# Performance work log

Measured on AMD Instinct MI355X. Metric: run time of the kernel, lower is better.

## Reference

```python
import jax, jax.numpy as jnp
import numpy as np

ND, NT, B = 16384, 16384, 4096
FD, FT, C = 256, 256, 768


def _gat(x_src, x_dst, ei, Ws, Wd, a_s, a_d, b, num_dst, self_loops):
    """PyG GATConv, heads=1: per-edge attention softmax over incoming edges."""
    if self_loops:
        loops = jnp.arange(num_dst, dtype=ei.dtype)
        ei = jnp.concatenate([ei, jnp.stack([loops, loops])], axis=1)
    src, dst = ei[0], ei[1]
    hs = x_src @ Ws                                   # [Ns, C]
    hd = x_dst @ Wd                                   # [Ndst, C]
    e = jax.nn.leaky_relu((hs @ a_s)[src] + (hd @ a_d)[dst], 0.2)   # [E]
    m = jax.ops.segment_max(e, dst, num_segments=num_dst)
    p = jnp.exp(e - m[dst])
    s = jax.ops.segment_sum(p, dst, num_segments=num_dst)
    alpha = p / (s[dst] + 1e-16)
    out = jax.ops.segment_sum(hs[src] * alpha[:, None], dst, num_segments=num_dst)
    return out + b


def _l2norm(x):
    n = jnp.linalg.norm(x, axis=1, keepdims=True)
    return x / jnp.maximum(n, 1e-12)


def setup_inputs() -> dict:
    ks = iter(jax.random.split(jax.random.key(0), 64))
    def nrm(shape, fan_in=None):
        s = 1.0 if fan_in is None else (1.0 / fan_in) ** 0.5
        return jax.random.normal(next(ks), shape, jnp.float32) * s
    inp = {}
    inp["x_drug"] = nrm((ND, FD))
    inp["x_target"] = nrm((NT, FT))
    inp["cell_features"] = nrm((B, 890))
    for et, fs, fd in (("dd", FD, FD), ("dt", FD, FT), ("tt", FT, FT)):
        inp[f"W_src_{et}"] = nrm((fs, C), fs)
        inp[f"W_dst_{et}"] = nrm((fd, C), fd)
        inp[f"a_src_{et}"] = nrm((C,), C)
        inp[f"a_dst_{et}"] = nrm((C,), C)
        inp[f"b_{et}"] = jnp.zeros((C,), jnp.float32)
    for name, fi, fo in (("red1", 890, 2048), ("red2", 2048, 512), ("red3", 512, 2 * C),
                         ("r2a", 4 * C, 2048), ("r2b", 2048, 512), ("r2c", 512, C), ("cls", C, 2)):
        inp[f"{name}_w"] = nrm((fi, fo), fi)
        inp[f"{name}_b"] = jnp.zeros((fo,), jnp.float32)
    inp["drug1_id"] = jax.random.randint(next(ks), (B,), 0, ND)
    inp["drug2_id"] = jax.random.randint(next(ks), (B,), 0, ND)
    inp["ei_dd"] = jax.random.randint(next(ks), (2, 131072), 0, ND)
    inp["ei_dt"] = jnp.stack([jax.random.randint(next(ks), (262144,), 0, ND),
                              jax.random.randint(next(ks), (262144,), 0, NT)])
    inp["ei_tt"] = jax.random.randint(next(ks), (2, 262144), 0, NT)
    return inp


def reference(x_drug, x_target, cell_features,
              W_src_dd, W_dst_dd, a_src_dd, a_dst_dd, b_dd,
              W_src_dt, W_dst_dt, a_src_dt, a_dst_dt, b_dt,
              W_src_tt, W_dst_tt, a_src_tt, a_dst_tt, b_tt,
              red1_w, red1_b, red2_w, red2_b, red3_w, red3_b,
              r2a_w, r2a_b, r2b_w, r2b_b, r2c_w, r2c_b,
              cls_w, cls_b,
              drug1_id, drug2_id, ei_dd, ei_dt, ei_tt):
    # HeteroConv (aggr='sum') followed by per-type ReLU, num_layers=1
    drug = jax.nn.relu(_gat(x_drug, x_drug, ei_dd,
                            W_src_dd, W_dst_dd, a_src_dd, a_dst_dd, b_dd, ND, True))
    target = jax.nn.relu(
        _gat(x_drug, x_target, ei_dt, W_src_dt, W_dst_dt, a_src_dt, a_dst_dt, b_dt, NT, False)
        + _gat(x_target, x_target, ei_tt, W_src_tt, W_dst_tt, a_src_tt, a_dst_tt, b_tt, NT, True))
    del target  # with num_layers=1 the target embeddings never feed the output (faithful)
    d1 = drug[drug1_id]
    d2 = drug[drug2_id]
    cell = _l2norm(cell_features)
    cell = jax.nn.relu(cell @ red1_w + red1_b)
    cell = jax.nn.relu(cell @ red2_w + red2_b)
    cell = jax.nn.relu(cell @ red3_w + red3_b)          # [B, 2*C]
    hidden = _l2norm(jnp.concatenate([d1, d2, cell], axis=1))  # [B, 4*C]
    hidden = jax.nn.relu(hidden @ r2a_w + r2a_b)
    hidden = jax.nn.relu(hidden @ r2b_w + r2b_b)
    hidden = jax.nn.relu(hidden @ r2c_w + r2c_b)
    return hidden @ cls_w + cls_b                       # [B, 2]
```

## Files before the change

### kernel.cpp

```cpp
#include <hip/hip_runtime.h>
#include <cstdint>

#define ND 16384
#define BATCH 4096
#define CDIM 768
#define E_DD 131072
#define FD 256

typedef unsigned short u16;
typedef u16 u16x4 __attribute__((ext_vector_type(4)));
typedef u16 u16x8 __attribute__((ext_vector_type(8)));
typedef short s16x8 __attribute__((ext_vector_type(8)));
typedef float f32x4 __attribute__((ext_vector_type(4)));

__device__ __forceinline__ u16 f2bf(float x) {
  union { float f; uint32_t u; } v; v.f = x;
  uint32_t r = v.u + 0x7fffu + ((v.u >> 16) & 1u);
  return (u16)(r >> 16);
}
__device__ __forceinline__ float bf2f(u16 h) {
  union { float f; uint32_t u; } v; v.u = ((uint32_t)h) << 16;
  return v.f;
}
__device__ __forceinline__ uint32_t split2p(float x) {
  u16 h = f2bf(x);
  u16 l = f2bf(x - bf2f(h));
  return ((uint32_t)h << 16) | l;
}

#define GLOAD_LDS16(gp, lp)                                                   \
  __builtin_amdgcn_global_load_lds(                                           \
      (__attribute__((address_space(1))) void*)(gp),                          \
      (__attribute__((address_space(3))) void*)(lp), 16, 0, 0)

__device__ __forceinline__ int xcd_chunk(int f, int nwg) {
  int q = nwg >> 3, r = nwg & 7;
  int xcd = f & 7, s = f >> 3;
  return (xcd < r ? xcd * (q + 1) : r * (q + 1) + (xcd - r) * q) + s;
}

#define KP 40

template <int KS, int OUT_BF16, int RELU, int BIAS, int ASPLIT, int ALO, int BLO,
          int BKD>
__device__ __forceinline__ void gemm_core(
    int bx, int by, int bz,
    const float* __restrict__ Af,
    const u16* __restrict__ Ahi, const u16* __restrict__ Alo,
    const u16* __restrict__ Bhi, const u16* __restrict__ Blo,
    const float* __restrict__ bias,
    float* __restrict__ Cf, u16* __restrict__ Chi,
    int M, int N, int K, u16* AsB, u16* BsB) {
  constexpr int MT = 4, NT = 4;
  constexpr int BM = 128, BN = 128;
  constexpr int ASEG = BM / 64;
  constexpr int BSEG = BN / 64;
  constexpr bool DIRECT = (ASPLIT == 0 && ALO == 0 && BLO == 0);

  const int t = threadIdx.x;
  const int bm0 = bx * BM, bn0 = by * BN;
  const int wid = t >> 6, lane = t & 63;
  const int quad = lane >> 4, l16 = lane & 15;
  const int wm0 = (wid >> 1) * (MT * 16);
  const int wn0 = (wid & 1) * (NT * 16);

  const int chunk = K / KS;
  const int kbeg = (KS > 1) ? bz * chunk : 0;
  const int kend = kbeg + chunk;

  float bvv[NT];
#pragma unroll
  for (int ni = 0; ni < NT; ++ni)
    bvv[ni] = BIAS ? bias[bn0 + wn0 + ni * 16 + l16] : 0.f;

  f32x4 acc[MT][NT];
#pragma unroll
  for (int i = 0; i < MT; ++i)
#pragma unroll
    for (int j = 0; j < NT; ++j) acc[i][j] = (f32x4){0.f, 0.f, 0.f, 0.f};

  if constexpr (DIRECT) {
    constexpr int SLOTS = BKD / 8;
    constexpr int SM = SLOTS - 1;
    constexpr int NLD = (BM * BKD) / (256 * 8);
    auto stageA = [&](int buf, int kk) {
#pragma unroll
      for (int c = 0; c < NLD; ++c) {
        int s = t + 256 * c;
        int r = s / SLOTS, j = s % SLOTS;
        int jj = j ^ (r & SM);
        size_t goff = (size_t)(bm0 + r) * K + kk + jj * 8;
        int lofs = __builtin_amdgcn_readfirstlane((wid * 64 + 256 * c) * 8);
        GLOAD_LDS16(Ahi + goff, AsB + buf * (BM * BKD) + lofs);
      }
    };
    auto stageB = [&](int buf, int kk) {
#pragma unroll
      for (int c = 0; c < NLD; ++c) {
        int s = t + 256 * c;
        int r = s / SLOTS, j = s % SLOTS;
        int jj = j ^ (r & SM);
        size_t goff = (size_t)(bn0 + r) * K + kk + jj * 8;
        int lofs = __builtin_amdgcn_readfirstlane((wid * 64 + 256 * c) * 8);
        GLOAD_LDS16(Bhi + goff, BsB + buf * (BN * BKD) + lofs);
      }
    };
    const int rsw = l16 & SM;
    stageA(0, kbeg);
    stageB(0, kbeg);
    int cur = 0;
    for (int k0 = kbeg;;) {
      __syncthreads();
      int kn = k0 + BKD;
      if (kn < kend) {
        stageA(cur ^ 1, kn);
        stageB(cur ^ 1, kn);
      }
      const u16* Ab = AsB + cur * (BM * BKD);
      const u16* Bb = BsB + cur * (BN * BKD);
#pragma unroll
      for (int h = 0; h < BKD / 32; ++h) {
        s16x8 ah[MT], bh[NT];
#pragma unroll
        for (int mi = 0; mi < MT; ++mi)
          ah[mi] = *(const s16x8*)(Ab + (wm0 + mi * 16 + l16) * BKD +
                                   (((h * 4 + quad) ^ rsw) * 8));
#pragma unroll
        for (int ni = 0; ni < NT; ++ni)
          bh[ni] = *(const s16x8*)(Bb + (wn0 + ni * 16 + l16) * BKD +
                                   (((h * 4 + quad) ^ rsw) * 8));
#pragma unroll
        for (int mi = 0; mi < MT; ++mi)
#pragma unroll
          for (int ni = 0; ni < NT; ++ni)
            acc[mi][ni] = __builtin_amdgcn_mfma_f32_16x16x32_bf16(
                ah[mi], bh[ni], acc[mi][ni], 0, 0, 0);
      }
      k0 = kn;
      cur ^= 1;
      if (k0 >= kend) break;
    }
  } else {
    auto As = [&](int a, int r, int k) -> u16& { return AsB[(a * BM + r) * KP + k]; };
    auto Bs = [&](int a, int r, int k) -> u16& { return BsB[(a * BN + r) * KP + k]; };

    u16x8 pAh[ASEG], pAl[ASEG], pBh[BSEG], pBl[BSEG];

    auto loadA = [&](int c, int kk) {
      int s = t + 256 * c, row = s >> 2, kq = (s & 3) * 8;
      size_t off = (size_t)(bm0 + row) * K + kk + kq;
      if (ASPLIT) {
        f32x4 v0 = *(const f32x4*)(Af + off);
        f32x4 v1 = *(const f32x4*)(Af + off + 4);
        u16x8 h, l;
#pragma unroll
        for (int e = 0; e < 4; ++e) {
          uint32_t p = split2p(v0[e]);
          h[e] = (u16)(p >> 16); l[e] = (u16)(p & 0xffffu);
          uint32_t q = split2p(v1[e]);
          h[e + 4] = (u16)(q >> 16); l[e + 4] = (u16)(q & 0xffffu);
        }
        pAh[c] = h; pAl[c] = l;
      } else {
        pAh[c] = *(const u16x8*)(Ahi + off);
        if (ALO) pAl[c] = *(const u16x8*)(Alo + off);
      }
    };
    auto loadB = [&](int c, int kk) {
      int s = t + 256 * c, row = s >> 2, kq = (s & 3) * 8;
      size_t off = (size_t)(bn0 + row) * K + kk + kq;
      pBh[c] = *(const u16x8*)(Bhi + off);
      if (BLO) pBl[c] = *(const u16x8*)(Blo + off);
    };

#pragma unroll
    for (int c = 0; c < ASEG; ++c) loadA(c, kbeg);
#pragma unroll
    for (int c = 0; c < BSEG; ++c) loadB(c, kbeg);

    for (int k0 = kbeg;;) {
      __syncthreads();
#pragma unroll
      for (int c = 0; c < ASEG; ++c) {
        int s = t + 256 * c, row = s >> 2, kq = (s & 3) * 8;
        *(u16x8*)&As(0, row, kq) = pAh[c];
        if (ALO) *(u16x8*)&As(1, row, kq) = pAl[c];
      }
#pragma unroll
      for (int c = 0; c < BSEG; ++c) {
        int s = t + 256 * c, row = s >> 2, kq = (s & 3) * 8;
        *(u16x8*)&Bs(0, row, kq) = pBh[c];
        if (BLO) *(u16x8*)&Bs(1, row, kq) = pBl[c];
      }
      __syncthreads();

      int kn = k0 + 32;
      if (kn < kend) {
#pragma unroll
        for (int c = 0; c < ASEG; ++c) loadA(c, kn);
#pragma unroll
        for (int c = 0; c < BSEG; ++c) loadB(c, kn);
      }

      s16x8 ah[MT], al[MT], bh[NT], bl[NT];
#pragma unroll
      for (int mi = 0; mi < MT; ++mi) {
        ah[mi] = *(const s16x8*)&As(0, wm0 + mi * 16 + l16, quad * 8);
        if (ALO) al[mi] = *(const s16x8*)&As(1, wm0 + mi * 16 + l16, quad * 8);
      }
#pragma unroll
      for (int ni = 0; ni < NT; ++ni) {
        bh[ni] = *(const s16x8*)&Bs(0, wn0 + ni * 16 + l16, quad * 8);
        if (BLO) bl[ni] = *(const s16x8*)&Bs(1, wn0 + ni * 16 + l16, quad * 8);
      }
#pragma unroll
      for (int mi = 0; mi < MT; ++mi)
#pragma unroll
        for (int ni = 0; ni < NT; ++ni) {
          acc[mi][ni] = __builtin_amdgcn_mfma_f32_16x16x32_bf16(
              ah[mi], bh[ni], acc[mi][ni], 0, 0, 0);
          if (BLO)
            acc[mi][ni] = __builtin_amdgcn_mfma_f32_16x16x32_bf16(
                ah[mi], bl[ni], acc[mi][ni], 0, 0, 0);
          if (ALO)
            acc[mi][ni] = __builtin_amdgcn_mfma_f32_16x16x32_bf16(
                al[mi], bh[ni], acc[mi][ni], 0, 0, 0);
        }
      k0 = kn;
      if (k0 >= kend) break;
    }
  }

  float* Cp = (KS > 1) ? Cf + (size_t)bz * M * N : Cf;
#pragma unroll
  for (int mi = 0; mi < MT; ++mi) {
#pragma unroll
    for (int ni = 0; ni < NT; ++ni) {
      int row = bm0 + wm0 + mi * 16 + quad * 4;
      int col = bn0 + wn0 + ni * 16 + l16;
#pragma unroll
      for (int r = 0; r < 4; ++r) {
        float v = acc[mi][ni][r] + bvv[ni];
        if (RELU) v = fmaxf(v, 0.f);
        size_t o = (size_t)(row + r) * N + col;
        if (OUT_BF16) Chi[o] = f2bf(v);
        else Cp[o] = v;
      }
    }
  }
}

template <int KS, int OUT_BF16, int RELU, int BIAS, int ASPLIT, int ALO, int BLO,
          int BKD>
__global__ __launch_bounds__(256) void mfma_gemm(
    const float* __restrict__ Af,
    const u16* __restrict__ Ahi, const u16* __restrict__ Alo,
    const u16* __restrict__ Bhi, const u16* __restrict__ Blo,
    const float* __restrict__ bias,
    float* __restrict__ Cf, u16* __restrict__ Chi,
    int M, int N, int K) {
  constexpr bool DIRECT = (ASPLIT == 0 && ALO == 0 && BLO == 0);
  __shared__ __align__(16) u16 AsB[DIRECT ? 2 * 128 * BKD : (ALO ? 2 : 1) * 128 * KP];
  __shared__ __align__(16) u16 BsB[DIRECT ? 2 * 128 * BKD : (BLO ? 2 : 1) * 128 * KP];
  int f = blockIdx.x + gridDim.x * blockIdx.y;
  int wg = xcd_chunk(f, gridDim.x * gridDim.y);
  int bx = wg % gridDim.x, by = wg / gridDim.x;
  gemm_core<KS, OUT_BF16, RELU, BIAS, ASPLIT, ALO, BLO, BKD>(
      bx, by, (KS > 1) ? (int)blockIdx.z : 0,
      Af, Ahi, Alo, Bhi, Blo, bias, Cf, Chi, M, N, K, AsB, BsB);
}

__device__ __forceinline__ void gat_body(
    int idx, int t,
    const u16* __restrict__ hs, const float* __restrict__ es,
    const float* __restrict__ ed, const int* __restrict__ offsets,
    const int* __restrict__ slots, const float* __restrict__ bias,
    const int* __restrict__ list, const int* __restrict__ cnt,
    u16* __restrict__ out) {
  if (idx >= *cnt) return;
  int d = list[idx];
  int lane = t & 63;
  int beg = offsets[d], end = offsets[d + 1];
  float edv = ed[d];
  float mx = -1e30f;
  for (int j = beg + lane; j < end; j += 64) {
    float e = es[slots[j]] + edv;
    e = e >= 0.f ? e : 0.2f * e;
    mx = fmaxf(mx, e);
  }
#pragma unroll
  for (int m = 32; m; m >>= 1) mx = fmaxf(mx, __shfl_xor(mx, m));
  float sm = 0.f;
  for (int j = beg + lane; j < end; j += 64) {
    float e = es[slots[j]] + edv;
    e = e >= 0.f ? e : 0.2f * e;
    sm += expf(e - mx);
  }
#pragma unroll
  for (int m = 32; m; m >>= 1) sm += __shfl_xor(sm, m);
  float inv = 1.f / (sm + 1e-16f);
  int c8 = lane * 8;
  int c4 = 512 + lane * 4;
  float a8[8] = {};
  float a4[4] = {};
  for (int j = beg; j < end; ++j) {
    int srcn = slots[j];
    float e = es[srcn] + edv;
    e = e >= 0.f ? e : 0.2f * e;
    float alpha = expf(e - mx) * inv;
    const u16* hrow = hs + (size_t)srcn * CDIM;
    u16x8 r8 = *(const u16x8*)(hrow + c8);
    u16x4 r4 = *(const u16x4*)(hrow + c4);
#pragma unroll
    for (int e2 = 0; e2 < 8; ++e2) a8[e2] = fmaf(alpha, bf2f(r8[e2]), a8[e2]);
#pragma unroll
    for (int e2 = 0; e2 < 4; ++e2) a4[e2] = fmaf(alpha, bf2f(r4[e2]), a4[e2]);
  }
  u16* orow = out + (size_t)d * CDIM;
  u16x8 o8;
  u16x4 o4;
#pragma unroll
  for (int e2 = 0; e2 < 8; ++e2) o8[e2] = f2bf(fmaxf(a8[e2] + bias[c8 + e2], 0.f));
#pragma unroll
  for (int e2 = 0; e2 < 4; ++e2) o4[e2] = f2bf(fmaxf(a4[e2] + bias[c4 + e2], 0.f));
  *(u16x8*)(orow + c8) = o8;
  *(u16x4*)(orow + c4) = o4;
}

__global__ __launch_bounds__(256) void gat_aggregate(
    const u16* __restrict__ hs, const float* __restrict__ es,
    const float* __restrict__ ed, const int* __restrict__ offsets,
    const int* __restrict__ slots, const float* __restrict__ bias,
    const int* __restrict__ list, const int* __restrict__ cnt,
    u16* __restrict__ out) {
  gat_body(blockIdx.x * 4 + (threadIdx.x >> 6), threadIdx.x,
           hs, es, ed, offsets, slots, bias, list, cnt, out);
}

__global__ __launch_bounds__(256) void dual_gemm_red1_hs_scatter(
    const u16* __restrict__ cn, const u16* __restrict__ r1T,
    const float* __restrict__ red1_b, u16* __restrict__ c1,
    const float* __restrict__ xd, const u16* __restrict__ wsrcT,
    u16* __restrict__ hs,
    const int* __restrict__ src, const int* __restrict__ dst,
    int* __restrict__ cursor, int* __restrict__ slots) {
  __shared__ __align__(16) u16 SMEM[16384];
  int b = blockIdx.x;
  if (b < 512) {
    int wg = xcd_chunk(b, 512);
    gemm_core<1, 1, 1, 1, 0, 0, 0, 32>(wg & 31, wg >> 5, 0, nullptr, cn, nullptr,
                                       r1T, nullptr, red1_b, nullptr, c1,
                                       BATCH, 2048, 896, SMEM, SMEM + 2 * 128 * 32);
  } else if (b < 1280) {
    int b2 = b - 512;
    gemm_core<1, 1, 0, 0, 1, 1, 0, 32>(b2 & 127, b2 >> 7, 0, xd, nullptr, nullptr,
                                       wsrcT, nullptr, nullptr, nullptr, hs,
                                       ND, CDIM, FD, SMEM, SMEM + 2 * 128 * KP);
  } else {
    int e = (b - 1280) * 256 + threadIdx.x;
    if (e < E_DD) {
      int pos = atomicAdd(&cursor[dst[e]], 1);
      slots[pos] = src[e];
    }
  }
}

template <int KS>
__global__ void reduce_split_ks(const float* __restrict__ P,
                                const float* __restrict__ bias,
                                u16* __restrict__ Chi, int M, int N) {
  int i = blockIdx.x * 256 + threadIdx.x;
  int total = (M * N) >> 2;
  if (i >= total) return;
  f32x4 s = ((const f32x4*)P)[i];
#pragma unroll
  for (int z = 1; z < KS; ++z) s += ((const f32x4*)P)[(size_t)z * total + i];
  int col = (i * 4) % N;
  f32x4 bv = *(const f32x4*)(bias + col);
  u16x4 h;
#pragma unroll
  for (int e = 0; e < 4; ++e) h[e] = f2bf(fmaxf(s[e] + bv[e], 0.f));
  *(u16x4*)&Chi[i * 4] = h;
}

__global__ void reduce_cls(const float* __restrict__ P,
                           const float* __restrict__ bias,
                           const float* __restrict__ clsw,
                           const float* __restrict__ clsb,
                           float* __restrict__ out) {
  int row = blockIdx.x * 4 + (threadIdx.x >> 6);
  int lane = threadIdx.x & 63;
  const f32x4* p0 = (const f32x4*)(P + (size_t)row * CDIM);
  const f32x4* p1 = (const f32x4*)(P + (size_t)BATCH * CDIM + (size_t)row * CDIM);
  float s0 = 0.f, s1 = 0.f;
#pragma unroll
  for (int i = 0; i < 3; ++i) {
    int c4 = lane + 64 * i;
    f32x4 a = p0[c4] + p1[c4];
    f32x4 bv = *(const f32x4*)(bias + c4 * 4);
#pragma unroll
    for (int e = 0; e < 4; ++e) {
      float h = fmaxf(a[e] + bv[e], 0.f);
      int c = c4 * 4 + e;
      s0 = fmaf(h, clsw[c * 2 + 0], s0);
      s1 = fmaf(h, clsw[c * 2 + 1], s1);
    }
  }
#pragma unroll
  for (int m = 32; m; m >>= 1) {
    s0 += __shfl_xor(s0, m);
    s1 += __shfl_xor(s1, m);
  }
  if (lane == 0) {
    out[row * 2 + 0] = s0 + clsb[0];
    out[row * 2 + 1] = s1 + clsb[1];
  }
}

struct TDesc {
  const float* W;
  u16* Th;
  int K, N, Kpad, start;
};
struct TPack { TDesc d[7]; };

#define P1_T 11328
#define P1_W (P1_T + 256)
#define P1_I (P1_W + 64)
__global__ __launch_bounds__(256) void prep1(
    TPack p,
    const float* __restrict__ Wsrc, const float* __restrict__ Wdst,
    const float* __restrict__ a_s, const float* __restrict__ a_d,
    float* __restrict__ wsv, float* __restrict__ wdv,
    int* __restrict__ counts, int* __restrict__ mask, int* __restrict__ cnt,
    const float* __restrict__ cellf, u16* __restrict__ cn_hi) {
  __shared__ __align__(16) float S[1088];
  int b = blockIdx.x;
  int t = threadIdx.x;
  if (b < P1_T) {
    float (*tile)[33] = (float(*)[33])S;
    int mi = 0;
#pragma unroll
    for (int i = 1; i < 7; ++i)
      if (b >= p.d[i].start) mi = i;
    TDesc dd = p.d[mi];
    int rel = b - dd.start;
    int tilesX = dd.Kpad / 32;
    int k0 = (rel % tilesX) * 32, n0 = (rel / tilesX) * 32;
    int tx = t & 31, ty = t >> 5;
#pragma unroll
    for (int i = 0; i < 4; ++i) {
      int k = k0 + ty + 8 * i, n = n0 + tx;
      tile[ty + 8 * i][tx] = (k < dd.K && n < dd.N) ? dd.W[(size_t)k * dd.N + n] : 0.f;
    }
    __syncthreads();
#pragma unroll
    for (int i = 0; i < 4; ++i) {
      int n = n0 + ty + 8 * i, k = k0 + tx;
      if (n < dd.N) dd.Th[(size_t)n * dd.Kpad + k] = f2bf(tile[tx][ty + 8 * i]);
    }
  } else if (b < P1_W) {
    int k = b - P1_T;
    float* rs = S;
    float* rd = S + 256;
    float s = 0.f, d = 0.f;
    for (int c = t; c < CDIM; c += 256) {
      s += Wsrc[(size_t)k * CDIM + c] * a_s[c];
      d += Wdst[(size_t)k * CDIM + c] * a_d[c];
    }
    rs[t] = s; rd[t] = d;
    __syncthreads();
    for (int st = 128; st; st >>= 1) {
      if (t < st) { rs[t] += rs[t + st]; rd[t] += rd[t + st]; }
      __syncthreads();
    }
    if (t == 0) { wsv[k] = rs[0]; wdv[k] = rd[0]; }
  } else if (b < P1_I) {
    int i = (b - P1_W) * 256 + t;
    if (i < ND) { counts[i] = 1; mask[i] = 0; }
    if (i == 0) *cnt = 0;
  } else {
    int row = b - P1_I;
    float* red = S;
    const float* irow = cellf + (size_t)row * 890;
    float s = 0.f;
    for (int c = t; c < 890; c += 256) { float v = irow[c]; s += v * v; }
    red[t] = s;
    __syncthreads();
    for (int st = 128; st; st >>= 1) {
      if (t < st) red[t] += red[t + st];
      __syncthreads();
    }
    float inv = 1.f / fmaxf(sqrtf(red[0]), 1e-12f);
    for (int c = t; c < 896; c += 256) {
      float v = (c < 890) ? irow[c] * inv : 0.f;
      cn_hi[(size_t)row * 896 + c] = f2bf(v);
    }
  }
}

#define P2_E (ND * FD / 1024)
#define P2_M (P2_E + BATCH / 256)
__global__ __launch_bounds__(256) void prep2(
    const float* __restrict__ x, const float* __restrict__ wsv,
    const float* __restrict__ wdv, float* __restrict__ es, float* __restrict__ ed,
    const int* __restrict__ d1, const int* __restrict__ d2, int* __restrict__ mask,
    const int* __restrict__ dst, int* __restrict__ counts) {
  int b = blockIdx.x, t = threadIdx.x;
  if (b < P2_E) {
    int i = b * 256 + t;
    int lane = t & 63;
    int row = i >> 6;
    int c4 = lane * 4;
    f32x4 v = ((const f32x4*)x)[i];
    f32x4 ws = *(const f32x4*)(wsv + c4);
    f32x4 wd = *(const f32x4*)(wdv + c4);
    float a = v[0] * ws[0] + v[1] * ws[1] + v[2] * ws[2] + v[3] * ws[3];
    float bb = v[0] * wd[0] + v[1] * wd[1] + v[2] * wd[2] + v[3] * wd[3];
#pragma unroll
    for (int m = 32; m; m >>= 1) {
      a += __shfl_xor(a, m);
      bb += __shfl_xor(bb, m);
    }
    if (lane == 0) { es[row] = a; ed[row] = bb; }
  } else if (b < P2_M) {
    int i = (b - P2_E) * 256 + t;
    mask[d1[i]] = 1;
    mask[d2[i]] = 1;
  } else {
    int e = (b - P2_M) * 256 + t;
    atomicAdd(&counts[dst[e]], 1);
  }
}

__global__ __launch_bounds__(512) void prep3(
    const int* __restrict__ mask, int* __restrict__ cnt, int* __restrict__ list,
    const int* __restrict__ counts, int* __restrict__ offsets,
    int* __restrict__ cursor, int* __restrict__ slots) {
  __shared__ int part[512];
  int b = blockIdx.x, t = threadIdx.x;
  if (b < 32) {
    int i = b * 512 + t;
    if (mask[i]) {
      int pos = atomicAdd(cnt, 1);
      list[pos] = i;
    }
  } else {
    int base = t * 32;
    int s = 0;
    for (int i = 0; i < 32; ++i) s += counts[base + i];
    part[t] = s;
    __syncthreads();
    if (t == 0) {
      int run = 0;
      for (int i = 0; i < 512; ++i) { int tmp = part[i]; part[i] = run; run += tmp; }
      offsets[ND] = run;
    }
    __syncthreads();
    int run = part[t];
    for (int i = 0; i < 32; ++i) {
      int d = base + i;
      offsets[d] = run;
      slots[run] = d;
      cursor[d] = run + 1;
      run += counts[d];
    }
  }
}

__global__ __launch_bounds__(256) void hidden_build_bf16(
    const u16* __restrict__ drug, const u16* __restrict__ c3,
    const int* __restrict__ d1, const int* __restrict__ d2,
    u16* __restrict__ hhi) {
  int row = blockIdx.x;
  int t = threadIdx.x;
  const u16* s1 = drug + (size_t)d1[row] * CDIM;
  const u16* s2 = drug + (size_t)d2[row] * CDIM;
  const u16* s3 = c3 + (size_t)row * (2 * CDIM);
  float vals[12];
  float ss = 0.f;
#pragma unroll
  for (int i = 0; i < 12; ++i) {
    int c = t + 256 * i;
    float v;
    if (i < 3)      v = bf2f(s1[c]);
    else if (i < 6) v = bf2f(s2[c - CDIM]);
    else            v = bf2f(s3[c - 2 * CDIM]);
    vals[i] = v;
    ss += v * v;
  }
  __shared__ float red[256];
  red[t] = ss;
  __syncthreads();
  for (int st = 128; st; st >>= 1) {
    if (t < st) red[t] += red[t + st];
    __syncthreads();
  }
  float inv = 1.f / fmaxf(sqrtf(red[0]), 1e-12f);
  u16* hrow_h = hhi + (size_t)row * (4 * CDIM);
#pragma unroll
  for (int i = 0; i < 12; ++i) hrow_h[t + 256 * i] = f2bf(vals[i] * inv);
}

extern "C" void kernel_launch(void* const* d_in, const int* in_sizes, int n_in,
                              void* d_out, int out_size, void* d_ws, size_t ws_size,
                              hipStream_t stream) {
  const float* x_drug   = (const float*)d_in[0];
  const float* cellf    = (const float*)d_in[2];
  const float* W_src_dd = (const float*)d_in[3];
  const float* W_dst_dd = (const float*)d_in[4];
  const float* a_src_dd = (const float*)d_in[5];
  const float* a_dst_dd = (const float*)d_in[6];
  const float* b_dd     = (const float*)d_in[7];
  const float* red1_w = (const float*)d_in[18];
  const float* red1_b = (const float*)d_in[19];
  const float* red2_w = (const float*)d_in[20];
  const float* red2_b = (const float*)d_in[21];
  const float* red3_w = (const float*)d_in[22];
  const float* red3_b = (const float*)d_in[23];
  const float* r2a_w  = (const float*)d_in[24];
  const float* r2a_b  = (const float*)d_in[25];
  const float* r2b_w  = (const float*)d_in[26];
  const float* r2b_b  = (const float*)d_in[27];
  const float* r2c_w  = (const float*)d_in[28];
  const float* r2c_b  = (const float*)d_in[29];
  const float* cls_w  = (const float*)d_in[30];
  const float* cls_b  = (const float*)d_in[31];
  const int* drug1_id = (const int*)d_in[32];
  const int* drug2_id = (const int*)d_in[33];
  const int* ei_dd    = (const int*)d_in[34];
  float* out = (float*)d_out;

  const int* dd_src = ei_dd;
  const int* dd_dst = ei_dd + E_DD;

  char* w = (char*)d_ws;
  size_t off = 0;
  auto alloc = [&](size_t bytes) -> char* {
    char* p = w + off;
    off = (off + bytes + 255) & ~(size_t)255;
    return p;
  };
  u16* hs   = (u16*)alloc((size_t)ND * CDIM * 2);
  u16* drug = (u16*)alloc((size_t)ND * CDIM * 2);
  u16* c3   = (u16*)alloc((size_t)BATCH * 2 * CDIM * 2);
  float* P  = (float*)alloc((size_t)4 * BATCH * 512 * 4);
  u16* hid_hi = hs;
  u16* cn_hi = (u16*)alloc((size_t)BATCH * 896 * 2);
  u16* c1_hi = (u16*)alloc((size_t)BATCH * 2048 * 2);
  u16* c2_hi = (u16*)alloc((size_t)BATCH * 512 * 2);
  u16* wsrcT_hi = (u16*)alloc((size_t)CDIM * FD * 2);
  u16* r1T_hi = (u16*)alloc((size_t)2048 * 896 * 2);
  u16* r2T_hi = (u16*)alloc((size_t)512 * 2048 * 2);
  u16* r3T_hi = (u16*)alloc((size_t)1536 * 512 * 2);
  u16* raT_hi = (u16*)alloc((size_t)2048 * 3072 * 2);
  u16* rbT_hi = (u16*)alloc((size_t)512 * 2048 * 2);
  u16* rcT_hi = (u16*)alloc((size_t)768 * 512 * 2);
  float* es  = (float*)alloc((size_t)ND * 4);
  float* ed  = (float*)alloc((size_t)ND * 4);
  float* wsv = (float*)alloc(FD * 4);
  float* wdv = (float*)alloc(FD * 4);
  int* counts  = (int*)alloc((size_t)ND * 4);
  int* offsets = (int*)alloc((size_t)(ND + 1) * 4);
  int* cursor  = (int*)alloc((size_t)ND * 4);
  int* slots   = (int*)alloc((size_t)(E_DD + ND) * 4);
  int* mask    = (int*)alloc((size_t)ND * 4);
  int* list    = (int*)alloc((size_t)ND * 4);
  int* cnt     = (int*)alloc(256);
  (void)ws_size; (void)n_in; (void)in_sizes; (void)out_size;

  TPack tp;
  tp.d[0] = {W_src_dd, wsrcT_hi, 256, 768, 256, 0};
  tp.d[1] = {red1_w, r1T_hi, 890, 2048, 896, 192};
  tp.d[2] = {red2_w, r2T_hi, 2048, 512, 2048, 1984};
  tp.d[3] = {red3_w, r3T_hi, 512, 1536, 512, 3008};
  tp.d[4] = {r2a_w, raT_hi, 3072, 2048, 3072, 3776};
  tp.d[5] = {r2b_w, rbT_hi, 2048, 512, 2048, 9920};
  tp.d[6] = {r2c_w, rcT_hi, 512, 768, 512, 10944};
  prep1<<<15744, 256, 0, stream>>>(tp, W_src_dd, W_dst_dd, a_src_dd, a_dst_dd,
                                   wsv, wdv, counts, mask, cnt, cellf, cn_hi);

  prep2<<<4624, 256, 0, stream>>>(x_drug, wsv, wdv, es, ed, drug1_id, drug2_id,
                                  mask, dd_dst, counts);

  prep3<<<33, 512, 0, stream>>>(mask, cnt, list, counts, offsets, cursor, slots);

  dual_gemm_red1_hs_scatter<<<1792, 256, 0, stream>>>(
      cn_hi, r1T_hi, red1_b, c1_hi, x_drug, wsrcT_hi, hs,
      dd_src, dd_dst, cursor, slots);

  mfma_gemm<4, 0, 0, 0, 0, 0, 0, 64><<<dim3(BATCH / 128, 512 / 128, 4), 256, 0, stream>>>(
      nullptr, c1_hi, nullptr, r2T_hi, nullptr, nullptr, P, nullptr, BATCH, 512, 2048);
  reduce_split_ks<4><<<BATCH * 512 / 1024, 256, 0, stream>>>(P, red2_b, c2_hi, BATCH, 512);
  mfma_gemm<1, 1, 1, 1, 0, 0, 0, 64><<<dim3(BATCH / 128, 1536 / 128), 256, 0, stream>>>(
      nullptr, c2_hi, nullptr, r3T_hi, nullptr, red3_b, nullptr, c3, BATCH, 1536, 512);

  gat_aggregate<<<ND / 4, 256, 0, stream>>>(hs, es, ed, offsets, slots, b_dd, list, cnt, drug);

  hidden_build_bf16<<<BATCH, 256, 0, stream>>>(drug, c3, drug1_id, drug2_id, hid_hi);

  mfma_gemm<1, 1, 1, 1, 0, 0, 0, 64><<<dim3(BATCH / 128, 2048 / 128), 256, 0, stream>>>(
      nullptr, hid_hi, nullptr, raT_hi, nullptr, r2a_b, nullptr, c1_hi, BATCH, 2048, 3072);
  mfma_gemm<4, 0, 0, 0, 0, 0, 0, 64><<<dim3(BATCH / 128, 512 / 128, 4), 256, 0, stream>>>(
      nullptr, c1_hi, nullptr, rbT_hi, nullptr, nullptr, P, nullptr, BATCH, 512, 2048);
  reduce_split_ks<4><<<BATCH * 512 / 1024, 256, 0, stream>>>(P, r2b_b, c2_hi, BATCH, 512);
  mfma_gemm<2, 0, 0, 0, 0, 0, 0, 64><<<dim3(BATCH / 128, CDIM / 128, 2), 256, 0, stream>>>(
      nullptr, c2_hi, nullptr, rcT_hi, nullptr, nullptr, P, nullptr, BATCH, CDIM, 512);
  reduce_cls<<<BATCH / 4, 256, 0, stream>>>(P, r2c_b, cls_w, cls_b, out);
}
```

Measured before the change: 452.3 us.

## Use 8-wave workgroups for standalone GEMMs and drop XCD tile remapping

Generalizes the GEMM core over the wave count, so standalone GEMM launches run 512 threads with 8 waves in a 2x4 layout, each wave computing a 64x32 sub-tile. This halves per-wave accumulator registers and spreads the staging loads across more threads, aiming for better latency hiding. It also removes the XCD-aware block-index remap from both the standalone and fused GEMMs and uses raw block indices instead. That can hurt L2 locality across chiplets, and each wave now reuses less data per fragment load.

```diff
diff --git a/kernel.cpp b/kernel.cpp
--- a/kernel.cpp
+++ b/kernel.cpp
@@ -33,16 +33,10 @@
       (__attribute__((address_space(1))) void*)(gp),                          \
       (__attribute__((address_space(3))) void*)(lp), 16, 0, 0)
 
-__device__ __forceinline__ int xcd_chunk(int f, int nwg) {
-  int q = nwg >> 3, r = nwg & 7;
-  int xcd = f & 7, s = f >> 3;
-  return (xcd < r ? xcd * (q + 1) : r * (q + 1) + (xcd - r) * q) + s;
-}
-
 #define KP 40
 
 template <int KS, int OUT_BF16, int RELU, int BIAS, int ASPLIT, int ALO, int BLO,
-          int BKD>
+          int BKD, int NW>
 __device__ __forceinline__ void gemm_core(
     int bx, int by, int bz,
     const float* __restrict__ Af,
@@ -51,7 +45,10 @@
     const float* __restrict__ bias,
     float* __restrict__ Cf, u16* __restrict__ Chi,
     int M, int N, int K, u16* AsB, u16* BsB) {
-  constexpr int MT = 4, NT = 4;
+  constexpr int NTH = NW * 64;
+  constexpr int WC = (NW == 8) ? 4 : 2;
+  constexpr int MT = 4;
+  constexpr int NT = (NW == 8) ? 2 : 4;
   constexpr int BM = 128, BN = 128;
   constexpr int ASEG = BM / 64;
   constexpr int BSEG = BN / 64;
@@ -61,8 +58,8 @@
   const int bm0 = bx * BM, bn0 = by * BN;
   const int wid = t >> 6, lane = t & 63;
   const int quad = lane >> 4, l16 = lane & 15;
-  const int wm0 = (wid >> 1) * (MT * 16);
-  const int wn0 = (wid & 1) * (NT * 16);
+  const int wm0 = (wid / WC) * (MT * 16);
+  const int wn0 = (wid % WC) * (NT * 16);
 
   const int chunk = K / KS;
   const int kbeg = (KS > 1) ? bz * chunk : 0;
@@ -82,26 +79,26 @@
   if constexpr (DIRECT) {
     constexpr int SLOTS = BKD / 8;
     constexpr int SM = SLOTS - 1;
-    constexpr int NLD = (BM * BKD) / (256 * 8);
+    constexpr int NLD = (BM * BKD) / (NTH * 8);
     auto stageA = [&](int buf, int kk) {
 #pragma unroll
       for (int c = 0; c < NLD; ++c) {
-        int s = t + 256 * c;
+        int s = t + NTH * c;
         int r = s / SLOTS, j = s % SLOTS;
         int jj = j ^ (r & SM);
         size_t goff = (size_t)(bm0 + r) * K + kk + jj * 8;
-        int lofs = __builtin_amdgcn_readfirstlane((wid * 64 + 256 * c) * 8);
+        int lofs = __builtin_amdgcn_readfirstlane((wid * 64 + NTH * c) * 8);
         GLOAD_LDS16(Ahi + goff, AsB + buf * (BM * BKD) + lofs);
       }
     };
     auto stageB = [&](int buf, int kk) {
 #pragma unroll
       for (int c = 0; c < NLD; ++c) {
-        int s = t + 256 * c;
+        int s = t + NTH * c;
         int r = s / SLOTS, j = s % SLOTS;
         int jj = j ^ (r & SM);
         size_t goff = (size_t)(bn0 + r) * K + kk + jj * 8;
-        int lofs = __builtin_amdgcn_readfirstlane((wid * 64 + 256 * c) * 8);
+        int lofs = __builtin_amdgcn_readfirstlane((wid * 64 + NTH * c) * 8);
         GLOAD_LDS16(Bhi + goff, BsB + buf * (BN * BKD) + lofs);
       }
     };
@@ -251,8 +248,8 @@
 }
 
 template <int KS, int OUT_BF16, int RELU, int BIAS, int ASPLIT, int ALO, int BLO,
-          int BKD>
-__global__ __launch_bounds__(256) void mfma_gemm(
+          int BKD, int NW>
+__global__ __launch_bounds__(NW * 64) void mfma_gemm(
     const float* __restrict__ Af,
     const u16* __restrict__ Ahi, const u16* __restrict__ Alo,
     const u16* __restrict__ Bhi, const u16* __restrict__ Blo,
@@ -262,11 +259,8 @@
   constexpr bool DIRECT = (ASPLIT == 0 && ALO == 0 && BLO == 0);
   __shared__ __align__(16) u16 AsB[DIRECT ? 2 * 128 * BKD : (ALO ? 2 : 1) * 128 * KP];
   __shared__ __align__(16) u16 BsB[DIRECT ? 2 * 128 * BKD : (BLO ? 2 : 1) * 128 * KP];
-  int f = blockIdx.x + gridDim.x * blockIdx.y;
-  int wg = xcd_chunk(f, gridDim.x * gridDim.y);
-  int bx = wg % gridDim.x, by = wg / gridDim.x;
-  gemm_core<KS, OUT_BF16, RELU, BIAS, ASPLIT, ALO, BLO, BKD>(
-      bx, by, (KS > 1) ? (int)blockIdx.z : 0,
+  gemm_core<KS, OUT_BF16, RELU, BIAS, ASPLIT, ALO, BLO, BKD, NW>(
+      blockIdx.x, blockIdx.y, (KS > 1) ? (int)blockIdx.z : 0,
       Af, Ahi, Alo, Bhi, Blo, bias, Cf, Chi, M, N, K, AsB, BsB);
 }
 
@@ -347,15 +341,14 @@
   __shared__ __align__(16) u16 SMEM[16384];
   int b = blockIdx.x;
   if (b < 512) {
-    int wg = xcd_chunk(b, 512);
-    gemm_core<1, 1, 1, 1, 0, 0, 0, 32>(wg & 31, wg >> 5, 0, nullptr, cn, nullptr,
-                                       r1T, nullptr, red1_b, nullptr, c1,
-                                       BATCH, 2048, 896, SMEM, SMEM + 2 * 128 * 32);
+    gemm_core<1, 1, 1, 1, 0, 0, 0, 32, 4>(b & 31, b >> 5, 0, nullptr, cn, nullptr,
+                                          r1T, nullptr, red1_b, nullptr, c1,
+                                          BATCH, 2048, 896, SMEM, SMEM + 2 * 128 * 32);
   } else if (b < 1280) {
     int b2 = b - 512;
-    gemm_core<1, 1, 0, 0, 1, 1, 0, 32>(b2 & 127, b2 >> 7, 0, xd, nullptr, nullptr,
-                                       wsrcT, nullptr, nullptr, nullptr, hs,
-                                       ND, CDIM, FD, SMEM, SMEM + 2 * 128 * KP);
+    gemm_core<1, 1, 0, 0, 1, 1, 0, 32, 4>(b2 & 127, b2 >> 7, 0, xd, nullptr, nullptr,
+                                          wsrcT, nullptr, nullptr, nullptr, hs,
+                                          ND, CDIM, FD, SMEM, SMEM + 2 * 128 * KP);
   } else {
     int e = (b - 1280) * 256 + threadIdx.x;
     if (e < E_DD) {
@@ -689,22 +682,22 @@
       cn_hi, r1T_hi, red1_b, c1_hi, x_drug, wsrcT_hi, hs,
       dd_src, dd_dst, cursor, slots);
 
-  mfma_gemm<4, 0, 0, 0, 0, 0, 0, 64><<<dim3(BATCH / 128, 512 / 128, 4), 256, 0, stream>>>(
+  mfma_gemm<4, 0, 0, 0, 0, 0, 0, 64, 8><<<dim3(BATCH / 128, 512 / 128, 4), 512, 0, stream>>>(
       nullptr, c1_hi, nullptr, r2T_hi, nullptr, nullptr, P, nullptr, BATCH, 512, 2048);
   reduce_split_ks<4><<<BATCH * 512 / 1024, 256, 0, stream>>>(P, red2_b, c2_hi, BATCH, 512);
-  mfma_gemm<1, 1, 1, 1, 0, 0, 0, 64><<<dim3(BATCH / 128, 1536 / 128), 256, 0, stream>>>(
+  mfma_gemm<1, 1, 1, 1, 0, 0, 0, 64, 8><<<dim3(BATCH / 128, 1536 / 128), 512, 0, stream>>>(
       nullptr, c2_hi, nullptr, r3T_hi, nullptr, red3_b, nullptr, c3, BATCH, 1536, 512);
 
   gat_aggregate<<<ND / 4, 256, 0, stream>>>(hs, es, ed, offsets, slots, b_dd, list, cnt, drug);
 
   hidden_build_bf16<<<BATCH, 256, 0, stream>>>(drug, c3, drug1_id, drug2_id, hid_hi);
 
-  mfma_gemm<1, 1, 1, 1, 0, 0, 0, 64><<<dim3(BATCH / 128, 2048 / 128), 256, 0, stream>>>(
+  mfma_gemm<1, 1, 1, 1, 0, 0, 0, 64, 8><<<dim3(BATCH / 128, 2048 / 128), 512, 0, stream>>>(
       nullptr, hid_hi, nullptr, raT_hi, nullptr, r2a_b, nullptr, c1_hi, BATCH, 2048, 3072);
-  mfma_gemm<4, 0, 0, 0, 0, 0, 0, 64><<<dim3(BATCH / 128, 512 / 128, 4), 256, 0, stream>>>(
+  mfma_gemm<4, 0, 0, 0, 0, 0, 0, 64, 8><<<dim3(BATCH / 128, 512 / 128, 4), 512, 0, stream>>>(
       nullptr, c1_hi, nullptr, rbT_hi, nullptr, nullptr, P, nullptr, BATCH, 512, 2048);
   reduce_split_ks<4><<<BATCH * 512 / 1024, 256, 0, stream>>>(P, r2b_b, c2_hi, BATCH, 512);
-  mfma_gemm<2, 0, 0, 0, 0, 0, 0, 64><<<dim3(BATCH / 128, CDIM / 128, 2), 256, 0, stream>>>(
+  mfma_gemm<2, 0, 0, 0, 0, 0, 0, 64, 8><<<dim3(BATCH / 128, CDIM / 128, 2), 512, 0, stream>>>(
       nullptr, c2_hi, nullptr, rcT_hi, nullptr, nullptr, P, nullptr, BATCH, CDIM, 512);
   reduce_cls<<<BATCH / 4, 256, 0, stream>>>(P, r2c_b, cls_w, cls_b, out);
 }
```

New measurement: 441.5 us (median of 2 runs). 2.4% less time.
